# Kernel optimization log

Measured on AMD Instinct MI355X. Metric: run time of the kernel, lower is better.

## Reference

```python
import jax, jax.numpy as jnp
import numpy as np

N_NODES = 100000
N_EDGES = 1600000
D = 64


def setup_inputs() -> dict:
    key = jax.random.key(0)
    k0, k1, k2, k3 = jax.random.split(key, 4)
    scale = 1.0 / np.sqrt(D)
    return {
        "x": jax.random.normal(k0, (N_NODES, D), dtype=jnp.float32),
        "W1": jax.random.normal(k1, (D, D), dtype=jnp.float32) * scale,
        "W2": jax.random.normal(k2, (D, D), dtype=jnp.float32) * scale,
        "b2": jnp.zeros((D,), dtype=jnp.float32),
        "edge_index": jax.random.randint(k3, (2, N_EDGES), 0, N_NODES, dtype=jnp.int32),
    }


def reference(x, W1, W2, b2, edge_index):
    # KapoorConv forward in eval mode (Dropout(p=0.5) is identity at inference).
    n = x.shape[0]
    # GCNConv adds self-loops, then symmetric normalization D^-1/2 A D^-1/2.
    loops = jnp.arange(n, dtype=edge_index.dtype)
    src = jnp.concatenate([edge_index[0], loops])  # message source j
    dst = jnp.concatenate([edge_index[1], loops])  # aggregation target i
    deg = jnp.zeros((n,), x.dtype).at[dst].add(jnp.float32(1.0))
    dinv = jax.lax.rsqrt(deg)  # deg >= 1 thanks to self-loops
    norm = (dinv[src] * dinv[dst])[:, None]  # [E+N, 1]

    def gcn(h, W, b):
        h = h @ W                                   # dense transform first
        msg = h[src] * norm                         # gather + normalize
        out = jax.ops.segment_sum(msg, dst, num_segments=n)  # scatter-add
        return out if b is None else out + b

    h = jax.nn.relu(gcn(x, W1, None))  # layer1: bias=False
    return gcn(h, W2, b2)              # layer2: bias=True
```

## Files before the change

### kernel.cpp

```cpp
#include <hip/hip_runtime.h>

#define D 64
#define CHUNK 4096
#define BKT_SHIFT 8
#define BKT_NODES 256
#define MAXB 512
#define CAP 8192
#define GROWS 64
#define SSTR 68

typedef unsigned int u32;

__device__ __forceinline__ u32 bfr(float v) {
    u32 x = __float_as_uint(v);
    return (x + 0x7fffu + ((x >> 16) & 1u)) >> 16;
}
__device__ __forceinline__ u32 pack2(float lo, float hi) { return bfr(lo) | (bfr(hi) << 16); }
__device__ __forceinline__ float blo(u32 w) { return __uint_as_float(w << 16); }
__device__ __forceinline__ float bhi(u32 w) { return __uint_as_float(w & 0xffff0000u); }


__global__ void partition(const int* __restrict__ src, const int* __restrict__ dst,
                          int* __restrict__ cursor, int* __restrict__ packed,
                          int nE, int B) {
    __shared__ int hist[MAXB];
    __shared__ int delta[MAXB];
    __shared__ int wsum[16];
    __shared__ int dstl[CHUNK];
    __shared__ int sorted[CHUNK];
    __shared__ unsigned short sortedb[CHUNK];
    int t = threadIdx.x;
    int i0 = blockIdx.x * CHUNK;
    int cn = min(CHUNK, nE - i0);

    if (t < MAXB) hist[t] = 0;
    __syncthreads();
    for (int i = t; i < cn; i += 1024) {
        int d = dst[i0 + i];
        dstl[i] = d;
        atomicAdd(&hist[d >> BKT_SHIFT], 1);
    }
    __syncthreads();

    int v = (t < MAXB) ? hist[t] : 0;
    int incl = v;
#pragma unroll
    for (int off = 1; off < 64; off <<= 1) {
        int u = __shfl_up(incl, off, 64);
        if ((t & 63) >= off) incl += u;
    }
    if ((t & 63) == 63 && t < MAXB) wsum[t >> 6] = incl;
    __syncthreads();
    if (t < MAXB) {
        int wp = 0;
        int w = t >> 6;
        for (int k = 0; k < w; ++k) wp += wsum[k];
        incl += wp;
        int excl = incl - v;
        int rb = 0;
        if (t < B && v > 0) rb = atomicAdd(&cursor[t], v);
        delta[t] = (t * CAP + rb) - excl;
        hist[t] = excl;
    }
    __syncthreads();

    for (int i = t; i < cn; i += 1024) {
        int d = dstl[i];
        int b = d >> BKT_SHIFT;
        int pp = atomicAdd(&hist[b], 1);
        sorted[pp]  = ((d & (BKT_NODES - 1)) << 17) | src[i0 + i];
        sortedb[pp] = (unsigned short)b;
    }
    __syncthreads();

    for (int i = t; i < cn; i += 1024) {
        packed[delta[sortedb[i]] + i] = sorted[i];
    }
}


__global__ void bucket_csr(const int* __restrict__ packed, const int* __restrict__ cursor,
                           int* __restrict__ row_ptr, float* __restrict__ dinv,
                           int* __restrict__ adj, const float* __restrict__ x,
                           u32* __restrict__ xp, int n, int B) {
    __shared__ int s[1024];
    __shared__ int hn[BKT_NODES];
    __shared__ int cur[BKT_NODES];
    __shared__ float dv[BKT_NODES];
    __shared__ int wsum[4];
    __shared__ int base_s;
    __shared__ int pk[CAP];
    int t = threadIdx.x;
    int b = blockIdx.x;
    int rlo = b * CAP;
    int mycnt = min(cursor[b], CAP);

    int partial = (t < b) ? cursor[t] : 0;
    s[t] = partial;
    __syncthreads();
    for (int off = 512; off > 0; off >>= 1) {
        if (t < off) s[t] += s[t + off];
        __syncthreads();
    }
    if (t == 0) base_s = s[0];
    __syncthreads();
    int base = base_s;
    if (b == B - 1 && t == 0) row_ptr[n] = base + mycnt;

    if (t < BKT_NODES) hn[t] = 0;
    __syncthreads();
    for (int i = t; i < mycnt; i += 1024) {
        int w = packed[rlo + i];
        pk[i] = w;
        atomicAdd(&hn[w >> 17], 1);
    }
    __syncthreads();

    int v = (t < BKT_NODES) ? hn[t] : 0;
    int incl = v;
#pragma unroll
    for (int off = 1; off < 64; off <<= 1) {
        int u = __shfl_up(incl, off, 64);
        if ((t & 63) >= off) incl += u;
    }
    if ((t & 63) == 63 && t < BKT_NODES) wsum[t >> 6] = incl;
    __syncthreads();
    if (t < BKT_NODES) {
        int wp = 0;
        int w = t >> 6;
        for (int k = 0; k < w; ++k) wp += wsum[k];
        incl += wp;
        int gbeg = base + incl - v;
        int node = (b << BKT_SHIFT) + t;
        float di = rsqrtf(1.0f + (float)v);
        if (node < n) {
            row_ptr[node] = gbeg;
            dinv[node] = di;
        }
        dv[t] = di;
        cur[t] = gbeg;
    }
    __syncthreads();

    for (int i = t; i < mycnt; i += 1024) {
        int w = pk[i];
        int pos = atomicAdd(&cur[w >> 17], 1);
        adj[pos] = w & 0x1FFFF;
    }

    int nbase = b << BKT_SHIFT;
    for (int i = t; i < BKT_NODES * 8; i += 1024) {
        int row = i >> 3, fb = i & 7;
        int nd = nbase + row;
        if (nd < n) {
            float d2 = dv[row];
            const float4* xr = (const float4*)(x + (size_t)nd * D + 8 * fb);
            float4 v0 = xr[0], v1 = xr[1];
            uint4 w;
            w.x = pack2(d2 * v0.x, d2 * v0.y);
            w.y = pack2(d2 * v0.z, d2 * v0.w);
            w.z = pack2(d2 * v1.x, d2 * v1.y);
            w.w = pack2(d2 * v1.z, d2 * v1.w);
            ((uint4*)(xp + (size_t)nd * (D / 2)))[fb] = w;
        }
    }
}

template <int MODE>
__launch_bounds__(256, 4)
__global__ void fused(const u32* __restrict__ hp, const int* __restrict__ row_ptr,
                      const int* __restrict__ adj,
                      const float* __restrict__ W, const float* __restrict__ bias,
                      const float* __restrict__ dinv,
                      float* __restrict__ outf, u32* __restrict__ outb, int n) {
    __shared__ float Wl[D * D];
    __shared__ float Sl[GROWS * SSTR];
    const int t = threadIdx.x;

    for (int i = t; i < D * D / 4; i += 256)
        ((float4*)Wl)[i] = ((const float4*)W)[i];

    const int R0 = blockIdx.x * GROWS;

    const int lane = t & 63;
    const int o = lane >> 3;
    const int f = lane & 7;
    const int wv = t >> 6;

#pragma unroll
    for (int r = 0; r < 2; ++r) {
        int row = wv * 16 + r * 8 + o;
        int nq = R0 + row;
        bool valid = nq < n;
        int nqc = valid ? nq : 0;
        int rb = row_ptr[nqc];
        int re = row_ptr[nqc + 1];
        int len = valid ? (re - rb) : 0;

        uint4 sw = ((const uint4*)(hp + (size_t)nqc * (D / 2)))[f];
        float acc[8];
        acc[0] = blo(sw.x); acc[1] = bhi(sw.x);
        acc[2] = blo(sw.y); acc[3] = bhi(sw.y);
        acc[4] = blo(sw.z); acc[5] = bhi(sw.z);
        acc[6] = blo(sw.w); acc[7] = bhi(sw.w);

        int lm = len;
        lm = max(lm, __shfl_xor(lm, 8, 64));
        lm = max(lm, __shfl_xor(lm, 16, 64));
        lm = max(lm, __shfl_xor(lm, 32, 64));

        for (int base = 0; base < lm; base += 16) {
            int rem = len - base;
            int ia = 0, ib = 0;
            if (f < rem)     ia = adj[rb + base + f];
            if (f + 8 < rem) ib = adj[rb + base + 8 + f];
            uint4 vv[16];
            {
                int ss[16];
#pragma unroll
                for (int u = 0; u < 8; ++u) {
                    ss[u]     = __shfl(ia, (o << 3) | u, 64);
                    ss[u + 8] = __shfl(ib, (o << 3) | u, 64);
                }
#pragma unroll
                for (int u = 0; u < 16; ++u) {
                    vv[u] = ((const uint4*)(hp + (size_t)ss[u] * (D / 2)))[f];
                }
            }
#pragma unroll
            for (int u = 0; u < 16; ++u) {
                float m = (u < rem) ? 1.0f : 0.0f;
                acc[0] = fmaf(m, blo(vv[u].x), acc[0]);
                acc[1] = fmaf(m, bhi(vv[u].x), acc[1]);
                acc[2] = fmaf(m, blo(vv[u].y), acc[2]);
                acc[3] = fmaf(m, bhi(vv[u].y), acc[3]);
                acc[4] = fmaf(m, blo(vv[u].z), acc[4]);
                acc[5] = fmaf(m, bhi(vv[u].z), acc[5]);
                acc[6] = fmaf(m, blo(vv[u].w), acc[6]);
                acc[7] = fmaf(m, bhi(vv[u].w), acc[7]);
            }
        }
        *(float4*)&Sl[row * SSTR + 8 * f]     = make_float4(acc[0], acc[1], acc[2], acc[3]);
        *(float4*)&Sl[row * SSTR + 8 * f + 4] = make_float4(acc[4], acc[5], acc[6], acc[7]);
    }
    __syncthreads();

    const int cg = t & 15;
    const int rg = t >> 4;

    float4 acc0 = make_float4(0.f, 0.f, 0.f, 0.f);
    float4 acc1 = make_float4(0.f, 0.f, 0.f, 0.f);
    float4 acc2 = make_float4(0.f, 0.f, 0.f, 0.f);
    float4 acc3 = make_float4(0.f, 0.f, 0.f, 0.f);

#pragma unroll 4
    for (int k = 0; k < D; k += 4) {
        float4 a0 = *(const float4*)&Sl[(4 * rg + 0) * SSTR + k];
        float4 a1 = *(const float4*)&Sl[(4 * rg + 1) * SSTR + k];
        float4 a2 = *(const float4*)&Sl[(4 * rg + 2) * SSTR + k];
        float4 a3 = *(const float4*)&Sl[(4 * rg + 3) * SSTR + k];
        float4 w0 = *(const float4*)&Wl[(k + 0) * D + 4 * cg];
        float4 w1 = *(const float4*)&Wl[(k + 1) * D + 4 * cg];
        float4 w2 = *(const float4*)&Wl[(k + 2) * D + 4 * cg];
        float4 w3 = *(const float4*)&Wl[(k + 3) * D + 4 * cg];
#define MAC(ACC, A)                                                        \
        ACC.x = fmaf(A.x, w0.x, fmaf(A.y, w1.x, fmaf(A.z, w2.x, fmaf(A.w, w3.x, ACC.x)))); \
        ACC.y = fmaf(A.x, w0.y, fmaf(A.y, w1.y, fmaf(A.z, w2.y, fmaf(A.w, w3.y, ACC.y)))); \
        ACC.z = fmaf(A.x, w0.z, fmaf(A.y, w1.z, fmaf(A.z, w2.z, fmaf(A.w, w3.z, ACC.z)))); \
        ACC.w = fmaf(A.x, w0.w, fmaf(A.y, w1.w, fmaf(A.z, w2.w, fmaf(A.w, w3.w, ACC.w))))
        MAC(acc0, a0);
        MAC(acc1, a1);
        MAC(acc2, a2);
        MAC(acc3, a3);
#undef MAC
    }

    const float4 bv = (MODE == 1) ? ((const float4*)bias)[cg]
                                  : make_float4(0.f, 0.f, 0.f, 0.f);
    float4 accs[4] = {acc0, acc1, acc2, acc3};
#pragma unroll
    for (int r = 0; r < 4; ++r) {
        int row = R0 + 4 * rg + r;
        if (row >= n) break;
        float dn = dinv[row];
        float4 y = accs[r];
        if (MODE == 0) {
            float o0 = dn * fmaxf(dn * y.x, 0.f);
            float o1 = dn * fmaxf(dn * y.y, 0.f);
            float o2 = dn * fmaxf(dn * y.z, 0.f);
            float o3 = dn * fmaxf(dn * y.w, 0.f);
            uint2 w2o;
            w2o.x = pack2(o0, o1);
            w2o.y = pack2(o2, o3);
            ((uint2*)(outb + (size_t)row * (D / 2)))[cg] = w2o;
        } else {
            float4 oo;
            oo.x = fmaf(dn, y.x, bv.x);
            oo.y = fmaf(dn, y.y, bv.y);
            oo.z = fmaf(dn, y.z, bv.z);
            oo.w = fmaf(dn, y.w, bv.w);
            ((float4*)(outf + (size_t)row * D))[cg] = oo;
        }
    }
}


extern "C" void kernel_launch(void* const* d_in, const int* in_sizes, int n_in,
                              void* d_out, int out_size, void* d_ws, size_t ws_size,
                              hipStream_t stream) {
    const float* x  = (const float*)d_in[0];
    const float* W1 = (const float*)d_in[1];
    const float* W2 = (const float*)d_in[2];
    const float* b2 = (const float*)d_in[3];
    const int*   ei = (const int*)d_in[4];

    int n  = in_sizes[0] / D;
    int nE = in_sizes[4] / 2;
    const int* src = ei;
    const int* dst = ei + nE;

    int B = (n + BKT_NODES - 1) >> BKT_SHIFT;

    auto align = [](size_t v) { return (v + 255) & ~(size_t)255; };
    char* ws = (char*)d_ws;
    size_t off = 0;
    int* row_ptr = (int*)(ws + off);   off += align((size_t)(n + 1) * 4);
    float* dinv  = (float*)(ws + off); off += align((size_t)n * 4);
    int* cursor  = (int*)(ws + off);   off += align((size_t)MAXB * 4);
    int* adj     = (int*)(ws + off);   off += align((size_t)nE * 4);
    int* packed  = (int*)(ws + off);   off += align((size_t)(B + 1) * CAP * 4);
    u32* F0      = (u32*)(ws + off);   off += align((size_t)n * (D / 2) * 4);
    u32* F1      = (u32*)(ws + off);
    float* out = (float*)d_out;

    int nchunks = (nE + CHUNK - 1) / CHUNK;

    hipMemsetAsync(cursor, 0, (size_t)MAXB * 4, stream);
    partition<<<nchunks, 1024, 0, stream>>>(src, dst, cursor, packed, nE, B);
    bucket_csr<<<B, 1024, 0, stream>>>(packed, cursor, row_ptr, dinv, adj, x, F0, n, B);

    int gblocks = (n + GROWS - 1) / GROWS;

    fused<0><<<gblocks, 256, 0, stream>>>(F0, row_ptr, adj, W1, nullptr, dinv, nullptr, F1, n);

    fused<1><<<gblocks, 256, 0, stream>>>(F1, row_ptr, adj, W2, b2, dinv, out, nullptr, n);
}
```

Measured before the change: 195.3 us.

## Sort nodes by degree bin to balance per-wave gather loop lengths

Adds a degree histogram in bucket_csr, a 64-bin scan and a permutation-fill kernel that orders nodes by in-degree. Both fused GCN kernels then process rows in that permuted order, so the 8 rows sharing a wave have similar neighbour counts and the max-length loop wastes fewer iterations. This costs two extra small launches, an extra indirection per row, and scattered output writes with less locality in row_ptr and the feature reads.

```diff
diff --git a/kernel.cpp b/kernel.cpp
--- a/kernel.cpp
+++ b/kernel.cpp
@@ -8,6 +8,7 @@
 #define CAP 8192
 #define GROWS 64
 #define SSTR 68
+#define NBIN 64
 
 typedef unsigned int u32;
 
@@ -82,12 +83,14 @@
 __global__ void bucket_csr(const int* __restrict__ packed, const int* __restrict__ cursor,
                            int* __restrict__ row_ptr, float* __restrict__ dinv,
                            int* __restrict__ adj, const float* __restrict__ x,
-                           u32* __restrict__ xp, int n, int B) {
+                           u32* __restrict__ xp, int* __restrict__ gBin,
+                           int* __restrict__ bo, int n, int B) {
     __shared__ int s[1024];
     __shared__ int hn[BKT_NODES];
     __shared__ int cur[BKT_NODES];
     __shared__ float dv[BKT_NODES];
     __shared__ int wsum[4];
+    __shared__ int dh[NBIN];
     __shared__ int base_s;
     __shared__ int pk[CAP];
     int t = threadIdx.x;
@@ -140,6 +143,15 @@
         dv[t] = di;
         cur[t] = gbeg;
     }
+
+    if (t < NBIN) dh[t] = 0;
+    __syncthreads();
+    if (t < BKT_NODES) {
+        int node = (b << BKT_SHIFT) + t;
+        if (node < n) atomicAdd(&dh[min(v, NBIN - 1)], 1);
+    }
+    __syncthreads();
+    if (t < NBIN) bo[b * NBIN + t] = atomicAdd(&gBin[t], dh[t]);
     __syncthreads();
 
     for (int i = t; i < mycnt; i += 1024) {
@@ -166,10 +178,37 @@
     }
 }
 
+__global__ void scan64(const int* __restrict__ gBin, int* __restrict__ binBase) {
+    int t = threadIdx.x;
+    int v = gBin[t];
+    int incl = v;
+#pragma unroll
+    for (int off = 1; off < 64; off <<= 1) {
+        int u = __shfl_up(incl, off, 64);
+        if (t >= off) incl += u;
+    }
+    binBase[t] = incl - v;
+}
+
+__global__ void perm_fill(const int* __restrict__ row_ptr, const int* __restrict__ binBase,
+                          const int* __restrict__ bo, int* __restrict__ perm, int n) {
+    __shared__ int lh[NBIN];
+    int t = threadIdx.x;
+    int b = blockIdx.x;
+    int node = b * BKT_NODES + t;
+    if (t < NBIN) lh[t] = 0;
+    __syncthreads();
+    if (node < n) {
+        int d = min(row_ptr[node + 1] - row_ptr[node], NBIN - 1);
+        int r = atomicAdd(&lh[d], 1);
+        perm[binBase[d] + bo[b * NBIN + d] + r] = node;
+    }
+}
+
 template <int MODE>
 __launch_bounds__(256, 4)
 __global__ void fused(const u32* __restrict__ hp, const int* __restrict__ row_ptr,
-                      const int* __restrict__ adj,
+                      const int* __restrict__ adj, const int* __restrict__ perm,
                       const float* __restrict__ W, const float* __restrict__ bias,
                       const float* __restrict__ dinv,
                       float* __restrict__ outf, u32* __restrict__ outb, int n) {
@@ -190,9 +229,10 @@
 #pragma unroll
     for (int r = 0; r < 2; ++r) {
         int row = wv * 16 + r * 8 + o;
-        int nq = R0 + row;
-        bool valid = nq < n;
-        int nqc = valid ? nq : 0;
+        int pr = R0 + row;
+        bool valid = pr < n;
+        int pri = valid ? pr : 0;
+        int nqc = perm[pri];
         int rb = row_ptr[nqc];
         int re = row_ptr[nqc + 1];
         int len = valid ? (re - rb) : 0;
@@ -280,9 +320,10 @@
     float4 accs[4] = {acc0, acc1, acc2, acc3};
 #pragma unroll
     for (int r = 0; r < 4; ++r) {
-        int row = R0 + 4 * rg + r;
-        if (row >= n) break;
-        float dn = dinv[row];
+        int pr = R0 + 4 * rg + r;
+        if (pr >= n) break;
+        int prow = perm[pr];
+        float dn = dinv[prow];
         float4 y = accs[r];
         if (MODE == 0) {
             float o0 = dn * fmaxf(dn * y.x, 0.f);
@@ -292,14 +333,14 @@
             uint2 w2o;
             w2o.x = pack2(o0, o1);
             w2o.y = pack2(o2, o3);
-            ((uint2*)(outb + (size_t)row * (D / 2)))[cg] = w2o;
+            ((uint2*)(outb + (size_t)prow * (D / 2)))[cg] = w2o;
         } else {
             float4 oo;
             oo.x = fmaf(dn, y.x, bv.x);
             oo.y = fmaf(dn, y.y, bv.y);
             oo.z = fmaf(dn, y.z, bv.z);
             oo.w = fmaf(dn, y.w, bv.w);
-            ((float4*)(outf + (size_t)row * D))[cg] = oo;
+            ((float4*)(outf + (size_t)prow * D))[cg] = oo;
         }
     }
 }
@@ -326,22 +367,29 @@
     size_t off = 0;
     int* row_ptr = (int*)(ws + off);   off += align((size_t)(n + 1) * 4);
     float* dinv  = (float*)(ws + off); off += align((size_t)n * 4);
-    int* cursor  = (int*)(ws + off);   off += align((size_t)MAXB * 4);
+    int* cursor  = (int*)(ws + off);   off += align((size_t)(MAXB + 2 * NBIN) * 4);
+    int* gBin    = cursor + MAXB;
+    int* binBase = cursor + MAXB + NBIN;
     int* adj     = (int*)(ws + off);   off += align((size_t)nE * 4);
     int* packed  = (int*)(ws + off);   off += align((size_t)(B + 1) * CAP * 4);
+    int* perm    = (int*)(ws + off);   off += align((size_t)n * 4);
+    int* bo      = (int*)(ws + off);   off += align((size_t)B * NBIN * 4);
     u32* F0      = (u32*)(ws + off);   off += align((size_t)n * (D / 2) * 4);
     u32* F1      = (u32*)(ws + off);
     float* out = (float*)d_out;
 
     int nchunks = (nE + CHUNK - 1) / CHUNK;
 
-    hipMemsetAsync(cursor, 0, (size_t)MAXB * 4, stream);
+    hipMemsetAsync(cursor, 0, (size_t)(MAXB + NBIN) * 4, stream);
     partition<<<nchunks, 1024, 0, stream>>>(src, dst, cursor, packed, nE, B);
-    bucket_csr<<<B, 1024, 0, stream>>>(packed, cursor, row_ptr, dinv, adj, x, F0, n, B);
+    bucket_csr<<<B, 1024, 0, stream>>>(packed, cursor, row_ptr, dinv, adj, x, F0,
+                                       gBin, bo, n, B);
+    scan64<<<1, 64, 0, stream>>>(gBin, binBase);
+    perm_fill<<<B, BKT_NODES, 0, stream>>>(row_ptr, binBase, bo, perm, n);
 
     int gblocks = (n + GROWS - 1) / GROWS;
 
-    fused<0><<<gblocks, 256, 0, stream>>>(F0, row_ptr, adj, W1, nullptr, dinv, nullptr, F1, n);
-
-    fused<1><<<gblocks, 256, 0, stream>>>(F1, row_ptr, adj, W2, b2, dinv, out, nullptr, n);
-}
+    fused<0><<<gblocks, 256, 0, stream>>>(F0, row_ptr, adj, perm, W1, nullptr, dinv, nullptr, F1, n);
+
+    fused<1><<<gblocks, 256, 0, stream>>>(F1, row_ptr, adj, perm, W2, b2, dinv, out, nullptr, n);
+}
```

Result: slower. 206.7 us (+5.9%).
